# Kernel tuning notes

Hardware: AMD Instinct MI355X
Metric: run time of the kernel (lower is better)

## Reference

```python
import jax, jax.numpy as jnp
import numpy as np


def setup_inputs() -> dict:
    key = jax.random.key(0)
    k1, k2 = jax.random.split(key)
    B, C, D = 16384, 4096, 1024
    feat = jax.random.normal(k1, (B, D), dtype=jnp.float32)
    centers = jax.random.normal(k2, (C, D), dtype=jnp.float32)
    return {"feat": feat, "centers": centers}


def reference(feat, centers):
    # Pairwise squared Euclidean distance: dist[b, c] = sum_d (feat[b,d] - centers[c,d])^2
    # materializing the O(B*C*D) broadcast difference (same math as the torch module).
    x2 = jnp.sum(feat * feat, axis=-1, keepdims=True)          # [B, 1]
    c2 = jnp.sum(centers * centers, axis=-1)[None, :]          # [1, C]
    xc = jnp.einsum("bd,cd->bc", feat, centers)                # [B, C] GEMM
    dist = x2 + c2 - 2.0 * xc
    return dist
```

## Files before the change

### kernel.cpp

```cpp
#include <hip/hip_runtime.h>
#include <hip/hip_bf16.h>

typedef __bf16 bf16x8 __attribute__((ext_vector_type(8)));
typedef float floatx4 __attribute__((ext_vector_type(4)));

__device__ __forceinline__ unsigned f2bf(float f) {
    unsigned u = __float_as_uint(f);
    u += 0x7FFFu + ((u >> 16) & 1u);
    return u >> 16;
}

__device__ __forceinline__ void gl2lds(const void* g, void* l) {
    void* gnc = const_cast<void*>(g);
    __builtin_amdgcn_global_load_lds(
        (__attribute__((address_space(1))) void*)gnc,
        (__attribute__((address_space(3))) void*)l,
        16, 0, 0);
}

__global__ __launch_bounds__(256) void cast_norm2(
    const float* __restrict__ feat, const float* __restrict__ cent,
    unsigned short* __restrict__ Ab, unsigned short* __restrict__ Bb,
    float* __restrict__ x2, float* __restrict__ c2, int M)
{
    const int tid  = threadIdx.x;
    const int half = tid >> 7;
    const int t    = tid & 127;
    const int row  = blockIdx.x * 2 + half;

    const float* src;
    unsigned short* dst;
    float* nrm;
    if (row < M) {
        src = feat + (size_t)row * 1024;
        dst = Ab   + (size_t)row * 1024;
        nrm = x2 + row;
    } else {
        const int r = row - M;
        src = cent + (size_t)r * 1024;
        dst = Bb   + (size_t)r * 1024;
        nrm = c2 + r;
    }

    const float4 v0 = ((const float4*)src)[t * 2];
    const float4 v1 = ((const float4*)src)[t * 2 + 1];
    float s = v0.x * v0.x + v0.y * v0.y + v0.z * v0.z + v0.w * v0.w
            + v1.x * v1.x + v1.y * v1.y + v1.z * v1.z + v1.w * v1.w;

    uint4 o;
    o.x = f2bf(v0.x) | (f2bf(v0.y) << 16);
    o.y = f2bf(v0.z) | (f2bf(v0.w) << 16);
    o.z = f2bf(v1.x) | (f2bf(v1.y) << 16);
    o.w = f2bf(v1.z) | (f2bf(v1.w) << 16);
    ((uint4*)dst)[t] = o;

#pragma unroll
    for (int off = 32; off > 0; off >>= 1) s += __shfl_down(s, off);
    __shared__ float ws[4];
    if ((tid & 63) == 0) ws[tid >> 6] = s;
    __syncthreads();
    if (t == 0) *nrm = ws[half * 2] + ws[half * 2 + 1];
}

__global__ __launch_bounds__(512, 2) void dist_gemm(
    const unsigned short* __restrict__ A,
    const unsigned short* __restrict__ B,
    const float* __restrict__ x2,
    const float* __restrict__ c2,
    float* __restrict__ out,
    int M, int N)
{
    __shared__ alignas(16) char lds_raw[131072];
    char* ldsb = lds_raw;
    const char* ldsc = lds_raw;

    const int tid  = threadIdx.x;
    const int wave = tid >> 6;
    const int lane = tid & 63;
    const int quad = lane >> 4;
    const int l16  = lane & 15;
    const int wm   = wave >> 2;
    const int wn   = wave & 3;

    const int gx  = gridDim.x;
    const int lin = blockIdx.y * gx + blockIdx.x;
    const int colsPerXcd = gx >> 3;
    const int xcd  = lin & 7;
    const int slot = lin >> 3;
    const int bx = xcd * colsPerXcd + (slot % colsPerXcd);
    const int by = slot / colsPerXcd;

    const int blockRow = by * 256;
    const int blockCol = bx * 256;

    const int cswz = (lane & 3) ^ (((lane >> 5) & 1) << 1);
    const unsigned short* pA = A + (size_t)(blockRow + wave * 16 + (lane >> 2)) * 1024 + cswz * 8;
    const unsigned short* pB = B + (size_t)(blockCol + wave * 16 + (lane >> 2)) * 1024 + cswz * 8;
    const int stOff = wave * 1024;

#define STAGE_A(buf, kt, h) do {                                              \
        const unsigned short* _s = pA + (size_t)(h) * 131072 + (kt) * 64;     \
        char* _d = ldsb + (buf) * 65536 + (h) * 8192 + stOff;                 \
        gl2lds(_s,      _d);                                                  \
        gl2lds(_s + 32, _d + 16384);                                          \
    } while (0)
#define STAGE_B(buf, kt, h) do {                                              \
        const unsigned short* _s = pB + (size_t)(h) * 131072 + (kt) * 64;     \
        char* _d = ldsb + (buf) * 65536 + 32768 + (h) * 8192 + stOff;         \
        gl2lds(_s,      _d);                                                  \
        gl2lds(_s + 32, _d + 16384);                                          \
    } while (0)

    const int swq = quad ^ ((l16 & 8) >> 2);
    const int aRd = (wm * 128 + l16) * 64 + swq * 16;
    const int bRd = 32768 + (wn * 64 + l16) * 64 + swq * 16;

#define RD_A(buf, ks, mf) (*(const bf16x8*)(ldsc + (buf) * 65536 + (ks) * 16384 + (mf) * 1024 + aRd))
#define RD_B(buf, ks, nf) (*(const bf16x8*)(ldsc + (buf) * 65536 + (ks) * 16384 + (nf) * 1024 + bRd))

#define LOAD_A8(arr, buf, ks) do {                                            \
        arr[0] = RD_A(buf, ks, 0); arr[1] = RD_A(buf, ks, 1);                 \
        arr[2] = RD_A(buf, ks, 2); arr[3] = RD_A(buf, ks, 3);                 \
        arr[4] = RD_A(buf, ks, 4); arr[5] = RD_A(buf, ks, 5);                 \
        arr[6] = RD_A(buf, ks, 6); arr[7] = RD_A(buf, ks, 7);                 \
    } while (0)
#define LOAD_B4(arr, buf, ks) do {                                            \
        arr[0] = RD_B(buf, ks, 0); arr[1] = RD_B(buf, ks, 1);                 \
        arr[2] = RD_B(buf, ks, 2); arr[3] = RD_B(buf, ks, 3);                 \
    } while (0)

#define BAR()    do { __builtin_amdgcn_s_barrier(); asm volatile("" ::: "memory"); } while (0)
#define LGKM0()  asm volatile("s_waitcnt lgkmcnt(0)" ::: "memory")
#define VMCNT4() asm volatile("s_waitcnt vmcnt(4)" ::: "memory")
#define VMCNT0() asm volatile("s_waitcnt vmcnt(0)" ::: "memory")

#define MFMA16(aa, mo, bb) do {                                               \
        __builtin_amdgcn_s_setprio(1);                                        \
        _Pragma("unroll")                                                     \
        for (int _m = 0; _m < 4; ++_m) {                                      \
            _Pragma("unroll")                                                 \
            for (int _n = 0; _n < 4; ++_n) {                                  \
                acc[(mo) + _m][_n] = __builtin_amdgcn_mfma_f32_16x16x32_bf16( \
                    aa[(mo) + _m], bb[_n], acc[(mo) + _m][_n], 0, 0, 0);      \
            }                                                                 \
        }                                                                     \
        __builtin_amdgcn_s_setprio(0);                                        \
    } while (0)

    floatx4 acc[8][4];
#pragma unroll
    for (int i = 0; i < 8; ++i)
#pragma unroll
        for (int j = 0; j < 4; ++j) acc[i][j] = (floatx4){0.f, 0.f, 0.f, 0.f};

    bf16x8 a0[8], a1[8], b0[4], b1[4];

    STAGE_A(0, 0, 0); STAGE_A(0, 0, 1);
    STAGE_B(0, 0, 0); STAGE_B(0, 0, 1);
    STAGE_A(1, 1, 0); STAGE_A(1, 1, 1);
    VMCNT4();
    BAR();

#define K_ITER(T, S) do {                                                     \
                                                                      \
        LOAD_A8(a0, 0, 0); LOAD_B4(b0, 0, 0);                                 \
        STAGE_B(1, (T) + 1, 0);                                               \
        BAR(); LGKM0(); MFMA16(a0, 0, b0); BAR();                             \
                                                                      \
        LOAD_A8(a1, 0, 1); LOAD_B4(b1, 0, 1);                                 \
        STAGE_B(1, (T) + 1, 1);                                               \
        BAR(); LGKM0(); MFMA16(a0, 4, b0); BAR();                             \
                                                                      \
        if (S) STAGE_A(0, (T) + 2, 0);                                        \
        BAR(); MFMA16(a1, 0, b1); BAR();                                      \
                                                                      \
        if (S) STAGE_A(0, (T) + 2, 1);                                        \
        BAR(); MFMA16(a1, 4, b1);                                             \
        if (S) { VMCNT4(); } else { VMCNT0(); }                               \
        BAR();                                                                \
                                                                      \
        LOAD_A8(a0, 1, 0); LOAD_B4(b0, 1, 0);                                 \
        if (S) STAGE_B(0, (T) + 2, 0);                                        \
        BAR(); LGKM0(); MFMA16(a0, 0, b0); BAR();                             \
                                                                      \
        LOAD_A8(a1, 1, 1); LOAD_B4(b1, 1, 1);                                 \
        if (S) STAGE_B(0, (T) + 2, 1);                                        \
        BAR(); LGKM0(); MFMA16(a0, 4, b0); BAR();                             \
                                                                      \
        if (S) STAGE_A(1, (T) + 3, 0);                                        \
        BAR(); MFMA16(a1, 0, b1); BAR();                                      \
                                                                      \
        if (S) STAGE_A(1, (T) + 3, 1);                                        \
        BAR(); MFMA16(a1, 4, b1); VMCNT4(); BAR();                            \
    } while (0)

#pragma unroll 1
    for (int it = 0; it < 7; ++it) {
        const int T = it * 2;
        K_ITER(T, true);
    }
    K_ITER(14, false);

    float c2v[4];
#pragma unroll
    for (int nf = 0; nf < 4; ++nf) c2v[nf] = c2[blockCol + wn * 64 + nf * 16 + l16];

#pragma unroll
    for (int mf = 0; mf < 8; ++mf) {
        const int rowb = blockRow + wm * 128 + mf * 16 + quad * 4;
        float x2v[4];
#pragma unroll
        for (int r = 0; r < 4; ++r) x2v[r] = x2[rowb + r];
#pragma unroll
        for (int nf = 0; nf < 4; ++nf) {
            const int col = blockCol + wn * 64 + nf * 16 + l16;
            float* o = out + (size_t)rowb * N + col;
#pragma unroll
            for (int r = 0; r < 4; ++r)
                o[(size_t)r * N] = fmaf(-2.0f, acc[mf][nf][r], x2v[r] + c2v[nf]);
        }
    }

#undef K_ITER
#undef MFMA16
#undef VMCNT0
#undef VMCNT4
#undef LGKM0
#undef BAR
#undef LOAD_B4
#undef LOAD_A8
#undef RD_B
#undef RD_A
#undef STAGE_B
#undef STAGE_A
}

__global__ __launch_bounds__(256) void dist_fallback(
    const float* __restrict__ A, const float* __restrict__ B,
    float* __restrict__ out, int M, int N, int K)
{
    __shared__ float sA[64][17];
    __shared__ float sB[64][17];
    const int tid = threadIdx.x;
    const int tx = tid & 15;
    const int ty = tid >> 4;
    const int rowBase = blockIdx.y * 64;
    const int colBase = blockIdx.x * 64;
    float acc[4][4] = {};
    for (int k0 = 0; k0 < K; k0 += 16) {
        __syncthreads();
        {
            const int r = tid >> 2, c = (tid & 3) * 4;
            float4 va = *(const float4*)(A + (size_t)(rowBase + r) * K + k0 + c);
            sA[r][c] = va.x; sA[r][c + 1] = va.y; sA[r][c + 2] = va.z; sA[r][c + 3] = va.w;
            float4 vb = *(const float4*)(B + (size_t)(colBase + r) * K + k0 + c);
            sB[r][c] = vb.x; sB[r][c + 1] = vb.y; sB[r][c + 2] = vb.z; sB[r][c + 3] = vb.w;
        }
        __syncthreads();
#pragma unroll
        for (int kk = 0; kk < 16; kk++) {
            float ra[4], rb[4];
#pragma unroll
            for (int i = 0; i < 4; i++) ra[i] = sA[ty * 4 + i][kk];
#pragma unroll
            for (int j = 0; j < 4; j++) rb[j] = sB[tx * 4 + j][kk];
#pragma unroll
            for (int i = 0; i < 4; i++)
#pragma unroll
                for (int j = 0; j < 4; j++) {
                    float d = ra[i] - rb[j];
                    acc[i][j] = fmaf(d, d, acc[i][j]);
                }
        }
    }
#pragma unroll
    for (int i = 0; i < 4; i++)
#pragma unroll
        for (int j = 0; j < 4; j++)
            out[(size_t)(rowBase + ty * 4 + i) * N + (colBase + tx * 4 + j)] = acc[i][j];
}

extern "C" void kernel_launch(void* const* d_in, const int* in_sizes, int n_in,
                              void* d_out, int out_size, void* d_ws, size_t ws_size,
                              hipStream_t stream) {
    const float* feat = (const float*)d_in[0];
    const float* cent = (const float*)d_in[1];
    float* out = (float*)d_out;

    const int D = 1024;
    const int M = in_sizes[0] / D;
    const int N = in_sizes[1] / D;

    const size_t offA  = 0;
    const size_t offB  = offA + (size_t)M * D * sizeof(unsigned short);
    const size_t offX2 = offB + (size_t)N * D * sizeof(unsigned short);
    const size_t offC2 = offX2 + (size_t)M * sizeof(float);
    const size_t need  = offC2 + (size_t)N * sizeof(float);

    if (ws_size >= need && (M % 256) == 0 && (N % 2048) == 0) {
        unsigned short* Ab = (unsigned short*)((char*)d_ws + offA);
        unsigned short* Bb = (unsigned short*)((char*)d_ws + offB);
        float* x2 = (float*)((char*)d_ws + offX2);
        float* c2 = (float*)((char*)d_ws + offC2);

        cast_norm2<<<(M + N) / 2, 256, 0, stream>>>(feat, cent, Ab, Bb, x2, c2, M);
        dist_gemm<<<dim3(N / 256, M / 256), 512, 0, stream>>>(Ab, Bb, x2, c2, out, M, N);
    } else {
        dist_fallback<<<dim3(N / 64, M / 64), 256, 0, stream>>>(feat, cent, out, M, N, D);
    }
}
```

Measured before the change: 430.8 us.

## Restructure GEMM K-loop to cut register use and simplify cast kernel per-wave

```diff
diff --git a/kernel.cpp b/kernel.cpp
--- a/kernel.cpp
+++ b/kernel.cpp
@@ -23,10 +23,9 @@
     unsigned short* __restrict__ Ab, unsigned short* __restrict__ Bb,
     float* __restrict__ x2, float* __restrict__ c2, int M)
 {
-    const int tid  = threadIdx.x;
-    const int half = tid >> 7;
-    const int t    = tid & 127;
-    const int row  = blockIdx.x * 2 + half;
+    const int wave = threadIdx.x >> 6;
+    const int lane = threadIdx.x & 63;
+    const int row  = blockIdx.x * 4 + wave;
 
     const float* src;
     unsigned short* dst;
@@ -42,24 +41,21 @@
         nrm = c2 + r;
     }
 
-    const float4 v0 = ((const float4*)src)[t * 2];
-    const float4 v1 = ((const float4*)src)[t * 2 + 1];
-    float s = v0.x * v0.x + v0.y * v0.y + v0.z * v0.z + v0.w * v0.w
-            + v1.x * v1.x + v1.y * v1.y + v1.z * v1.z + v1.w * v1.w;
-
-    uint4 o;
-    o.x = f2bf(v0.x) | (f2bf(v0.y) << 16);
-    o.y = f2bf(v0.z) | (f2bf(v0.w) << 16);
-    o.z = f2bf(v1.x) | (f2bf(v1.y) << 16);
-    o.w = f2bf(v1.z) | (f2bf(v1.w) << 16);
-    ((uint4*)dst)[t] = o;
-
+    const float4* s4 = (const float4*)src;
+    uint2* d2 = (uint2*)dst;
+    float s = 0.f;
+#pragma unroll
+    for (int j = 0; j < 4; ++j) {
+        const float4 v = s4[j * 64 + lane];
+        s += v.x * v.x + v.y * v.y + v.z * v.z + v.w * v.w;
+        uint2 o;
+        o.x = f2bf(v.x) | (f2bf(v.y) << 16);
+        o.y = f2bf(v.z) | (f2bf(v.w) << 16);
+        d2[j * 64 + lane] = o;
+    }
 #pragma unroll
     for (int off = 32; off > 0; off >>= 1) s += __shfl_down(s, off);
-    __shared__ float ws[4];
-    if ((tid & 63) == 0) ws[tid >> 6] = s;
-    __syncthreads();
-    if (t == 0) *nrm = ws[half * 2] + ws[half * 2 + 1];
+    if (lane == 0) *nrm = s;
 }
 
 __global__ __launch_bounds__(512, 2) void dist_gemm(
@@ -98,11 +94,14 @@
     const unsigned short* pB = B + (size_t)(blockCol + wave * 16 + (lane >> 2)) * 1024 + cswz * 8;
     const int stOff = wave * 1024;
 
-#define STAGE_A(buf, kt, h) do {                                              \
-        const unsigned short* _s = pA + (size_t)(h) * 131072 + (kt) * 64;     \
-        char* _d = ldsb + (buf) * 65536 + (h) * 8192 + stOff;                 \
-        gl2lds(_s,      _d);                                                  \
-        gl2lds(_s + 32, _d + 16384);                                          \
+#define STAGE_A(buf, kt) do {                                                 \
+        const unsigned short* _s0 = pA + (size_t)(kt) * 64;                   \
+        const unsigned short* _s1 = _s0 + 131072;                             \
+        char* _d0 = ldsb + (buf) * 65536 + stOff;                             \
+        gl2lds(_s0,      _d0);                                                \
+        gl2lds(_s0 + 32, _d0 + 16384);                                        \
+        gl2lds(_s1,      _d0 + 8192);                                         \
+        gl2lds(_s1 + 32, _d0 + 8192 + 16384);                                 \
     } while (0)
 #define STAGE_B(buf, kt, h) do {                                              \
         const unsigned short* _s = pB + (size_t)(h) * 131072 + (kt) * 64;     \
@@ -118,15 +117,15 @@
 #define RD_A(buf, ks, mf) (*(const bf16x8*)(ldsc + (buf) * 65536 + (ks) * 16384 + (mf) * 1024 + aRd))
 #define RD_B(buf, ks, nf) (*(const bf16x8*)(ldsc + (buf) * 65536 + (ks) * 16384 + (nf) * 1024 + bRd))
 
-#define LOAD_A8(arr, buf, ks) do {                                            \
-        arr[0] = RD_A(buf, ks, 0); arr[1] = RD_A(buf, ks, 1);                 \
-        arr[2] = RD_A(buf, ks, 2); arr[3] = RD_A(buf, ks, 3);                 \
-        arr[4] = RD_A(buf, ks, 4); arr[5] = RD_A(buf, ks, 5);                 \
-        arr[6] = RD_A(buf, ks, 6); arr[7] = RD_A(buf, ks, 7);                 \
-    } while (0)
-#define LOAD_B4(arr, buf, ks) do {                                            \
-        arr[0] = RD_B(buf, ks, 0); arr[1] = RD_B(buf, ks, 1);                 \
-        arr[2] = RD_B(buf, ks, 2); arr[3] = RD_B(buf, ks, 3);                 \
+#define LDA8(buf, mo) do {                                                    \
+        aF[0] = RD_A(buf, 0, (mo) + 0); aF[2] = RD_A(buf, 0, (mo) + 1);       \
+        aF[4] = RD_A(buf, 0, (mo) + 2); aF[6] = RD_A(buf, 0, (mo) + 3);       \
+        aF[1] = RD_A(buf, 1, (mo) + 0); aF[3] = RD_A(buf, 1, (mo) + 1);       \
+        aF[5] = RD_A(buf, 1, (mo) + 2); aF[7] = RD_A(buf, 1, (mo) + 3);       \
+    } while (0)
+#define LDB4(bb, buf, no) do {                                                \
+        bb[0] = RD_B(buf, 0, (no) + 0); bb[2] = RD_B(buf, 0, (no) + 1);       \
+        bb[1] = RD_B(buf, 1, (no) + 0); bb[3] = RD_B(buf, 1, (no) + 1);       \
     } while (0)
 
 #define BAR()    do { __builtin_amdgcn_s_barrier(); asm volatile("" ::: "memory"); } while (0)
@@ -134,14 +133,19 @@
 #define VMCNT4() asm volatile("s_waitcnt vmcnt(4)" ::: "memory")
 #define VMCNT0() asm volatile("s_waitcnt vmcnt(0)" ::: "memory")
 
-#define MFMA16(aa, mo, bb) do {                                               \
+#define MFMA_Q(mo, no, bb) do {                                               \
         __builtin_amdgcn_s_setprio(1);                                        \
         _Pragma("unroll")                                                     \
         for (int _m = 0; _m < 4; ++_m) {                                      \
             _Pragma("unroll")                                                 \
-            for (int _n = 0; _n < 4; ++_n) {                                  \
-                acc[(mo) + _m][_n] = __builtin_amdgcn_mfma_f32_16x16x32_bf16( \
-                    aa[(mo) + _m], bb[_n], acc[(mo) + _m][_n], 0, 0, 0);      \
+            for (int _n = 0; _n < 2; ++_n) {                                  \
+                _Pragma("unroll")                                             \
+                for (int _k = 0; _k < 2; ++_k) {                              \
+                    acc[(mo) + _m][(no) + _n] =                               \
+                        __builtin_amdgcn_mfma_f32_16x16x32_bf16(              \
+                            aF[_m * 2 + _k], bb[_n * 2 + _k],                 \
+                            acc[(mo) + _m][(no) + _n], 0, 0, 0);              \
+                }                                                             \
             }                                                                 \
         }                                                                     \
         __builtin_amdgcn_s_setprio(0);                                        \
@@ -153,53 +157,41 @@
 #pragma unroll
         for (int j = 0; j < 4; ++j) acc[i][j] = (floatx4){0.f, 0.f, 0.f, 0.f};
 
-    bf16x8 a0[8], a1[8], b0[4], b1[4];
-
-    STAGE_A(0, 0, 0); STAGE_A(0, 0, 1);
+    bf16x8 aF[8], bL[4], bH[4];
+
+#define HALF(buf, obuf, tB, tA, SB, SA, LASTVM) do {                          \
+                                                                      \
+        LDA8(buf, 0); LDB4(bL, buf, 0);                                       \
+        if (SB) STAGE_B(obuf, tB, 0);                                         \
+        BAR(); LGKM0(); MFMA_Q(0, 0, bL); BAR();                              \
+                                                                      \
+        LDB4(bH, buf, 2);                                                     \
+        if (SB) STAGE_B(obuf, tB, 1);                                         \
+        BAR(); LGKM0(); MFMA_Q(0, 2, bH); BAR();                              \
+                                                                      \
+        LDA8(buf, 4);                                                         \
+        BAR(); LGKM0(); MFMA_Q(4, 2, bH); BAR();                              \
+                                                                      \
+        if (SA) STAGE_A(buf, tA);                                             \
+        BAR(); MFMA_Q(4, 0, bL);                                              \
+        if (SA) { VMCNT4(); } else { LASTVM; }                                \
+        BAR();                                                                \
+    } while (0)
+
+    STAGE_A(0, 0);
     STAGE_B(0, 0, 0); STAGE_B(0, 0, 1);
-    STAGE_A(1, 1, 0); STAGE_A(1, 1, 1);
+    STAGE_A(1, 1);
     VMCNT4();
     BAR();
-
-#define K_ITER(T, S) do {                                                     \
-                                                                      \
-        LOAD_A8(a0, 0, 0); LOAD_B4(b0, 0, 0);                                 \
-        STAGE_B(1, (T) + 1, 0);                                               \
-        BAR(); LGKM0(); MFMA16(a0, 0, b0); BAR();                             \
-                                                                      \
-        LOAD_A8(a1, 0, 1); LOAD_B4(b1, 0, 1);                                 \
-        STAGE_B(1, (T) + 1, 1);                                               \
-        BAR(); LGKM0(); MFMA16(a0, 4, b0); BAR();                             \
-                                                                      \
-        if (S) STAGE_A(0, (T) + 2, 0);                                        \
-        BAR(); MFMA16(a1, 0, b1); BAR();                                      \
-                                                                      \
-        if (S) STAGE_A(0, (T) + 2, 1);                                        \
-        BAR(); MFMA16(a1, 4, b1);                                             \
-        if (S) { VMCNT4(); } else { VMCNT0(); }                               \
-        BAR();                                                                \
-                                                                      \
-        LOAD_A8(a0, 1, 0); LOAD_B4(b0, 1, 0);                                 \
-        if (S) STAGE_B(0, (T) + 2, 0);                                        \
-        BAR(); LGKM0(); MFMA16(a0, 0, b0); BAR();                             \
-                                                                      \
-        LOAD_A8(a1, 1, 1); LOAD_B4(b1, 1, 1);                                 \
-        if (S) STAGE_B(0, (T) + 2, 1);                                        \
-        BAR(); LGKM0(); MFMA16(a0, 4, b0); BAR();                             \
-                                                                      \
-        if (S) STAGE_A(1, (T) + 3, 0);                                        \
-        BAR(); MFMA16(a1, 0, b1); BAR();                                      \
-                                                                      \
-        if (S) STAGE_A(1, (T) + 3, 1);                                        \
-        BAR(); MFMA16(a1, 4, b1); VMCNT4(); BAR();                            \
-    } while (0)
 
 #pragma unroll 1
     for (int it = 0; it < 7; ++it) {
         const int T = it * 2;
-        K_ITER(T, true);
-    }
-    K_ITER(14, false);
+        HALF(0, 1, T + 1, T + 2, true, true, (void)0);
+        HALF(1, 0, T + 2, T + 3, true, true, (void)0);
+    }
+    HALF(0, 1, 15, 0, true, false, VMCNT0());
+    HALF(1, 0, 0, 0, false, false, (void)0);
 
     float c2v[4];
 #pragma unroll
@@ -221,14 +213,14 @@
         }
     }
 
-#undef K_ITER
-#undef MFMA16
+#undef HALF
+#undef MFMA_Q
 #undef VMCNT0
 #undef VMCNT4
 #undef LGKM0
 #undef BAR
-#undef LOAD_B4
-#undef LOAD_A8
+#undef LDB4
+#undef LDA8
 #undef RD_B
 #undef RD_A
 #undef STAGE_B
@@ -303,7 +295,7 @@
         float* x2 = (float*)((char*)d_ws + offX2);
         float* c2 = (float*)((char*)d_ws + offC2);
 
-        cast_norm2<<<(M + N) / 2, 256, 0, stream>>>(feat, cent, Ab, Bb, x2, c2, M);
+        cast_norm2<<<(M + N) / 4, 256, 0, stream>>>(feat, cent, Ab, Bb, x2, c2, M);
         dist_gemm<<<dim3(N / 256, M / 256), 512, 0, stream>>>(Ab, Bb, x2, c2, out, M, N);
     } else {
         dist_fallback<<<dim3(N / 64, M / 64), 256, 0, stream>>>(feat, cent, out, M, N, D);
```

New measurement: 430.6 us. About the same (-0.0%).
